# Kernel optimization log

Measured on AMD Instinct MI355X. Metric: run time of the kernel, lower is better.

Reference implementation:

```python
import jax, jax.numpy as jnp
import numpy as np
import math

D_MODEL = 1024
N_HEADS = 16
D_K = D_MODEL // N_HEADS
LN_EPS = 1e-5


def _linear_params(key, d_in, d_out):
    # torch Linear stores weight as [out, in]; xavier_uniform init
    bound = math.sqrt(6.0 / (d_in + d_out))
    kw, kb = jax.random.split(key)
    W = jax.random.uniform(kw, (d_out, d_in), jnp.float32, -bound, bound)
    b = jnp.zeros((d_out,), jnp.float32)
    return W, b


def setup_inputs() -> dict:
    key = jax.random.key(0)
    ks = jax.random.split(key, 8)
    x = jax.random.normal(ks[0], (2, 2048, D_MODEL), jnp.float32)
    reasoning_state = jax.random.normal(ks[1], (2, D_MODEL), jnp.float32)
    Wq, bq = _linear_params(ks[2], D_MODEL, D_MODEL)
    Wk, bk = _linear_params(ks[3], D_MODEL, D_MODEL)
    Wv, bv = _linear_params(ks[4], D_MODEL, D_MODEL)
    Wr, br = _linear_params(ks[5], D_MODEL, D_MODEL)
    Wo, bo = _linear_params(ks[6], D_MODEL, D_MODEL)
    ln_g = jnp.ones((D_MODEL,), jnp.float32)
    ln_b = jnp.zeros((D_MODEL,), jnp.float32)
    return {"x": x, "reasoning_state": reasoning_state,
            "Wq": Wq, "bq": bq, "Wk": Wk, "bk": bk, "Wv": Wv, "bv": bv,
            "Wr": Wr, "br": br, "Wo": Wo, "bo": bo, "ln_g": ln_g, "ln_b": ln_b}


def reference(x, reasoning_state, Wq, bq, Wk, bk, Wv, bv, Wr, br, Wo, bo, ln_g, ln_b):
    B, S, D = x.shape
    H, dk = N_HEADS, D_K

    def proj(z, W, b):  # torch Linear: z @ W.T + b
        return z @ W.T + b

    # [B, H, S, dk]
    Q = proj(x, Wq, bq).reshape(B, S, H, dk).transpose(0, 2, 1, 3)
    K = proj(x, Wk, bk).reshape(B, S, H, dk).transpose(0, 2, 1, 3)
    V = proj(x, Wv, bv).reshape(B, S, H, dk).transpose(0, 2, 1, 3)

    scores = jnp.einsum('bhsd,bhtd->bhst', Q, K) / math.sqrt(dk)

    # reasoning bias: R is [B, H, 1, dk]; Q @ R^T -> [B, H, S, 1], broadcast over keys
    R = proj(reasoning_state, Wr, br).reshape(B, 1, H, dk).transpose(0, 2, 1, 3)
    scores = scores + jnp.einsum('bhsd,bhud->bhsu', Q, R)  # u == 1, broadcasts

    attn = jax.nn.softmax(scores, axis=-1)
    context = jnp.einsum('bhst,bhtd->bshd', attn, V).reshape(B, S, D)
    out = proj(context, Wo, bo)

    # residual + LayerNorm
    y = out + x
    mu = jnp.mean(y, axis=-1, keepdims=True)
    var = jnp.var(y, axis=-1, keepdims=True)
    y = (y - mu) * jax.lax.rsqrt(var + LN_EPS) * ln_g + ln_b
    return (y, attn)
```

## Files before the change

### kernel.cpp

```cpp
#include <hip/hip_runtime.h>
#include <hip/hip_bf16.h>

#define DM 1024
#define NH 16
#define DKK 64
#define SL 2048
#define NBATCH 2
#define NR (NBATCH*SL)

typedef __attribute__((ext_vector_type(8))) __bf16 bf16x8;
typedef __attribute__((ext_vector_type(4))) float f32x4;
using bf16 = __hip_bfloat16;

#define QSCALE 0.18033688011112042f

__global__ __launch_bounds__(256) void cvt5_kernel(
    const float* __restrict__ sx, const float* __restrict__ s1,
    const float* __restrict__ s2, const float* __restrict__ s3, const float* __restrict__ s4,
    bf16* __restrict__ dx, bf16* __restrict__ d1,
    bf16* __restrict__ d2, bf16* __restrict__ d3, bf16* __restrict__ d4) {
  const int z = blockIdx.y;
  const float* src = (z == 0) ? sx : (z == 1) ? s1 : (z == 2) ? s2 : (z == 3) ? s3 : s4;
  bf16* dst = (z == 0) ? dx : (z == 1) ? d1 : (z == 2) ? d2 : (z == 3) ? d3 : d4;
  const int n4 = (z == 0) ? (NR * DM / 4) : (DM * DM / 4);
  int stride = gridDim.x * blockDim.x;
  for (int i = blockIdx.x * blockDim.x + threadIdx.x; i < n4; i += stride) {
    float4 v = ((const float4*)src)[i];
    union { bf16 h[4]; ushort4 u; } un;
    un.h[0] = __float2bfloat16(v.x);
    un.h[1] = __float2bfloat16(v.y);
    un.h[2] = __float2bfloat16(v.z);
    un.h[3] = __float2bfloat16(v.w);
    ((ushort4*)dst)[i] = un.u;
  }
}

__global__ __launch_bounds__(256) void gemm_qkv_kernel(
    const bf16* __restrict__ xb,
    const bf16* __restrict__ Wqb, const bf16* __restrict__ Wkb, const bf16* __restrict__ Wvb,
    const float* __restrict__ bq, const float* __restrict__ bk, const float* __restrict__ bv,
    bf16* __restrict__ Qb, bf16* __restrict__ Kb, bf16* __restrict__ Vt) {
  __shared__ bf16 smem[8192];
  bf16* As = smem;
  bf16* Bs = smem + 4096;
  const int z = blockIdx.z;
  const bf16* W = (z == 0) ? Wqb : (z == 1) ? Wkb : Wvb;
  const float* bias = (z == 0) ? bq : (z == 1) ? bk : bv;
  const int rowStart = blockIdx.y * 128, colStart = blockIdx.x * 64;
  const int t = threadIdx.x, lane = t & 63, w = t >> 6;
  const int lg = lane & 15, lh = lane >> 4;
  const int wm = (w >> 1) * 64, wn = (w & 1) * 32;

  f32x4 acc[4][2];
#pragma unroll
  for (int i = 0; i < 4; ++i)
#pragma unroll
    for (int j = 0; j < 2; ++j) acc[i][j] = (f32x4){0.f, 0.f, 0.f, 0.f};

  for (int kt = 0; kt < DM / 32; ++kt) {
    int kb = kt * 32;
#pragma unroll
    for (int q = 0; q < 2; ++q) {
      int idx = q * 256 + t;
      int row = idx >> 2;
      int ce = (idx & 3) * 8;
      const bf16* ga = xb + (size_t)(rowStart + row) * DM + kb + ce;
      int ldsbase = (q * 256 + w * 64) * 8;
      __builtin_amdgcn_global_load_lds((const __attribute__((address_space(1))) void*)ga,
                                       (__attribute__((address_space(3))) void*)(As + ldsbase),
                                       16, 0, 0);
    }
    {
      int row = t >> 2, ce = (t & 3) * 8;
      const bf16* gb = W + (size_t)(colStart + row) * DM + kb + ce;
      int ldsbase = (w * 64) * 8;
      __builtin_amdgcn_global_load_lds((const __attribute__((address_space(1))) void*)gb,
                                       (__attribute__((address_space(3))) void*)(Bs + ldsbase),
                                       16, 0, 0);
    }
    __syncthreads();
    bf16x8 af[4], bfr[2];
#pragma unroll
    for (int i = 0; i < 4; ++i)
      af[i] = *(const bf16x8*)(As + (wm + i * 16 + lg) * 32 + 8 * lh);
#pragma unroll
    for (int j = 0; j < 2; ++j)
      bfr[j] = *(const bf16x8*)(Bs + (wn + j * 16 + lg) * 32 + 8 * lh);
#pragma unroll
    for (int i = 0; i < 4; ++i)
#pragma unroll
      for (int j = 0; j < 2; ++j)
        acc[i][j] = __builtin_amdgcn_mfma_f32_16x16x32_bf16(af[i], bfr[j], acc[i][j], 0, 0, 0);
    __syncthreads();
  }

  if (z < 2) {
    bf16* out = (z == 0) ? Qb : Kb;
    const float sc = (z == 0) ? QSCALE : 1.0f;
#pragma unroll
    for (int i = 0; i < 4; ++i)
#pragma unroll
      for (int j = 0; j < 2; ++j) {
        int col = colStart + wn + j * 16 + lg;
        float bb = bias[col];
#pragma unroll
        for (int r = 0; r < 4; ++r) {
          int row = rowStart + wm + i * 16 + 4 * lh + r;
          out[(size_t)row * DM + col] = __float2bfloat16((acc[i][j][r] + bb) * sc);
        }
      }
  } else {
    char* T = (char*)smem;
    __syncthreads();
#pragma unroll
    for (int i = 0; i < 4; ++i)
#pragma unroll
      for (int j = 0; j < 2; ++j) {
        int col = wn + j * 16 + lg;
        float bb = bias[colStart + col];
        const int swz = (col & 7) << 4;
#pragma unroll
        for (int r2 = 0; r2 < 4; r2 += 2) {
          int row = wm + i * 16 + 4 * lh + r2;
          union { bf16 hh[2]; unsigned u; } un;
          un.hh[0] = __float2bfloat16(acc[i][j][r2] + bb);
          un.hh[1] = __float2bfloat16(acc[i][j][r2 + 1] + bb);
          *(unsigned*)(T + ((col * 256 + row * 2) ^ swz)) = un.u;
        }
      }
    __syncthreads();
    const int b_i = rowStart >> 11;
    const int sbase = rowStart & 2047;
#pragma unroll
    for (int rd = 0; rd < 4; ++rd) {
      int d_loc = rd * 16 + (t >> 4);
      int s8 = (t & 15) * 8;
      bf16x8 v = *(const bf16x8*)(T + ((d_loc * 256 + s8 * 2) ^ ((d_loc & 7) << 4)));
      int col = colStart + d_loc;
      int h2 = col >> 6, d = col & 63;
      *(bf16x8*)(Vt + ((size_t)(b_i * NH + h2) * DKK + d) * SL + sbase + s8) = v;
    }
  }
}

__global__ __launch_bounds__(256) void attn_den_kernel(
    const bf16* __restrict__ Qb, const bf16* __restrict__ Kb,
    float* __restrict__ linv_g) {
  __shared__ float sl[2 * 128];
  const int t = threadIdx.x, lane = t & 63, w = t >> 6;
  const int lg = lane & 15, lh = lane >> 4;
  const int L = blockIdx.x;
  const int xcd = L & 7, s_in = L >> 3;
  const int bh = xcd * 4 + (s_in >> 4);
  const int qtile = s_in & 15;
  const int b = bh >> 4, h = bh & 15;
  const int qbase = qtile * 128;
  const int wr = w >> 1, wc = w & 1;

  bf16x8 qf[4][2];
#pragma unroll
  for (int i = 0; i < 4; ++i)
#pragma unroll
    for (int ks = 0; ks < 2; ++ks)
      qf[i][ks] = *(const bf16x8*)(Qb +
          (size_t)(b * SL + qbase + wr * 64 + i * 16 + lg) * DM + h * DKK + ks * 32 + 8 * lh);

  const bf16* Kbase = Kb + (size_t)b * SL * DM + h * DKK;

  float lsum[4] = {0.f, 0.f, 0.f, 0.f};
  for (int kt = 0; kt < 16; ++kt) {
    bf16x8 kf[4][2];
#pragma unroll
    for (int j = 0; j < 4; ++j)
#pragma unroll
      for (int ks = 0; ks < 2; ++ks)
        kf[j][ks] = *(const bf16x8*)(Kbase +
            (size_t)(kt * 128 + wc * 64 + j * 16 + lg) * DM + ks * 32 + 8 * lh);
#pragma unroll
    for (int i = 0; i < 4; ++i) {
      f32x4 s[4];
#pragma unroll
      for (int j = 0; j < 4; ++j) {
        f32x4 z = (f32x4){0.f, 0.f, 0.f, 0.f};
        z = __builtin_amdgcn_mfma_f32_16x16x32_bf16(kf[j][0], qf[i][0], z, 0, 0, 0);
        s[j] = __builtin_amdgcn_mfma_f32_16x16x32_bf16(kf[j][1], qf[i][1], z, 0, 0, 0);
      }
#pragma unroll
      for (int j = 0; j < 4; ++j)
#pragma unroll
        for (int r = 0; r < 4; ++r) lsum[i] += exp2f(s[j][r]);
    }
  }
#pragma unroll
  for (int i = 0; i < 4; ++i) {
    lsum[i] += __shfl_xor(lsum[i], 16);
    lsum[i] += __shfl_xor(lsum[i], 32);
  }
  if (lh == 0) {
#pragma unroll
    for (int i = 0; i < 4; ++i) sl[wc * 128 + wr * 64 + i * 16 + lg] = lsum[i];
  }
  __syncthreads();
  if (t < 128) {
    linv_g[(size_t)bh * SL + qbase + t] = 1.f / (sl[t] + sl[128 + t]);
  }
}

__global__ __launch_bounds__(256) void attn_wr_kernel(
    const bf16* __restrict__ Qb, const bf16* __restrict__ Kb, const bf16* __restrict__ Vt,
    const float* __restrict__ linv_g,
    float* __restrict__ attn_out, bf16* __restrict__ ctxb) {
  __shared__ bf16 Ps[4][2][32 * 128];
  const int t = threadIdx.x, lane = t & 63, w = t >> 6;
  const int lg = lane & 15, lh = lane >> 4;
  const int L = blockIdx.x;
  const int xcd = L & 7, s_in = L >> 3;
  const int bh = xcd * 4 + (s_in >> 4);
  const int qtile = s_in & 15;
  const int b = bh >> 4, h = bh & 15;
  const int qb2 = qtile * 128 + w * 32;
  char* Pw = (char*)(&Ps[w][0][0]);

  bf16x8 qf[2][2];
#pragma unroll
  for (int i = 0; i < 2; ++i)
#pragma unroll
    for (int ks = 0; ks < 2; ++ks)
      qf[i][ks] = *(const bf16x8*)(Qb +
          (size_t)(b * SL + qb2 + i * 16 + lg) * DM + h * DKK + ks * 32 + 8 * lh);

  float linv[2];
#pragma unroll
  for (int i = 0; i < 2; ++i)
    linv[i] = linv_g[(size_t)bh * SL + qb2 + i * 16 + lg];

  const bf16* Kbase = Kb + (size_t)b * SL * DM + h * DKK;
  const bf16* Vtb = Vt + (size_t)bh * DKK * SL;
  float* attn_base = attn_out + (size_t)bh * SL * SL;

  f32x4 cacc[2][4];
#pragma unroll
  for (int i = 0; i < 2; ++i)
#pragma unroll
    for (int jd = 0; jd < 4; ++jd) cacc[i][jd] = (f32x4){0.f, 0.f, 0.f, 0.f};

  for (int kt = 0; kt < 16; ++kt) {
    char* Pb = Pw + (kt & 1) * 8192;
    bf16x8 kf[8][2];
#pragma unroll
    for (int j = 0; j < 8; ++j)
#pragma unroll
      for (int ks = 0; ks < 2; ++ks)
        kf[j][ks] = *(const bf16x8*)(Kbase +
            (size_t)(kt * 128 + j * 16 + lg) * DM + ks * 32 + 8 * lh);
    bf16x8 vfall[4][4];
#pragma unroll
    for (int ks = 0; ks < 4; ++ks)
#pragma unroll
      for (int jd = 0; jd < 4; ++jd)
        vfall[ks][jd] = *(const bf16x8*)(Vtb +
            (size_t)(jd * 16 + lg) * SL + kt * 128 + ks * 32 + 8 * lh);

#pragma unroll
    for (int i = 0; i < 2; ++i) {
      f32x4 s[8];
      __builtin_amdgcn_s_setprio(1);
#pragma unroll
      for (int j = 0; j < 8; ++j) {
        f32x4 z = (f32x4){0.f, 0.f, 0.f, 0.f};
        z = __builtin_amdgcn_mfma_f32_16x16x32_bf16(kf[j][0], qf[i][0], z, 0, 0, 0);
        s[j] = __builtin_amdgcn_mfma_f32_16x16x32_bf16(kf[j][1], qf[i][1], z, 0, 0, 0);
      }
      __builtin_amdgcn_s_setprio(0);
      const int qloc = i * 16 + lg;
      const int swz = (qloc & 7) << 4;
#pragma unroll
      for (int j = 0; j < 8; ++j) {
        const int key0 = j * 16 + 4 * lh;
        f32x4 p4;
        p4[0] = exp2f(s[j][0]) * linv[i];
        p4[1] = exp2f(s[j][1]) * linv[i];
        p4[2] = exp2f(s[j][2]) * linv[i];
        p4[3] = exp2f(s[j][3]) * linv[i];
        __builtin_nontemporal_store(p4,
            (f32x4*)(attn_base + (size_t)(qb2 + qloc) * SL + kt * 128 + key0));
        union { bf16 hh[4]; ushort4 u4; } un;
        un.hh[0] = __float2bfloat16(p4[0]);
        un.hh[1] = __float2bfloat16(p4[1]);
        un.hh[2] = __float2bfloat16(p4[2]);
        un.hh[3] = __float2bfloat16(p4[3]);
        *(ushort4*)(Pb + ((qloc * 256 + key0 * 2) ^ swz)) = un.u4;
      }
    }

    __builtin_amdgcn_s_setprio(1);
#pragma unroll
    for (int ks = 0; ks < 4; ++ks) {
      bf16x8 pf[2];
#pragma unroll
      for (int i = 0; i < 2; ++i) {
        const int qloc = i * 16 + lg;
        pf[i] = *(const bf16x8*)(Pb + ((qloc * 256 + (ks * 32 + 8 * lh) * 2) ^ ((qloc & 7) << 4)));
      }
#pragma unroll
      for (int i = 0; i < 2; ++i)
#pragma unroll
        for (int jd = 0; jd < 4; ++jd)
          cacc[i][jd] = __builtin_amdgcn_mfma_f32_16x16x32_bf16(pf[i], vfall[ks][jd], cacc[i][jd], 0, 0, 0);
    }
    __builtin_amdgcn_s_setprio(0);
  }

#pragma unroll
  for (int i = 0; i < 2; ++i)
#pragma unroll
    for (int jd = 0; jd < 4; ++jd)
#pragma unroll
      for (int r = 0; r < 4; ++r) {
        int row = qb2 + i * 16 + 4 * lh + r;
        int d = jd * 16 + lg;
        ctxb[(size_t)(b * SL + row) * DM + h * DKK + d] = __float2bfloat16(cacc[i][jd][r]);
      }
}

__global__ __launch_bounds__(256) void gemm_o_kernel(
    const bf16* __restrict__ ctxb, const bf16* __restrict__ Wob, const float* __restrict__ bo,
    const float* __restrict__ xf, float* __restrict__ ypre) {
  __shared__ bf16 As[128 * 32], Bs[64 * 32];
  const int t = threadIdx.x, lane = t & 63, w = t >> 6;
  const int lg = lane & 15, lh = lane >> 4;
  const int wm = (w >> 1) * 64, wn = (w & 1) * 32;
  int rowStart = blockIdx.y * 128, colStart = blockIdx.x * 64;
  f32x4 acc[4][2];
#pragma unroll
  for (int i = 0; i < 4; ++i)
#pragma unroll
    for (int j = 0; j < 2; ++j) acc[i][j] = (f32x4){0.f, 0.f, 0.f, 0.f};

  for (int kt = 0; kt < DM / 32; ++kt) {
    int kb = kt * 32;
#pragma unroll
    for (int q = 0; q < 2; ++q) {
      int idx = q * 256 + t;
      int row = idx >> 2;
      int ce = (idx & 3) * 8;
      const bf16* ga = ctxb + (size_t)(rowStart + row) * DM + kb + ce;
      int ldsbase = (q * 256 + w * 64) * 8;
      __builtin_amdgcn_global_load_lds((const __attribute__((address_space(1))) void*)ga,
                                       (__attribute__((address_space(3))) void*)(As + ldsbase),
                                       16, 0, 0);
    }
    {
      int row = t >> 2, ce = (t & 3) * 8;
      const bf16* gb = Wob + (size_t)(colStart + row) * DM + kb + ce;
      int ldsbase = (w * 64) * 8;
      __builtin_amdgcn_global_load_lds((const __attribute__((address_space(1))) void*)gb,
                                       (__attribute__((address_space(3))) void*)(Bs + ldsbase),
                                       16, 0, 0);
    }
    __syncthreads();
    bf16x8 af[4], bfr[2];
#pragma unroll
    for (int i = 0; i < 4; ++i)
      af[i] = *(const bf16x8*)(As + (wm + i * 16 + lg) * 32 + 8 * lh);
#pragma unroll
    for (int j = 0; j < 2; ++j)
      bfr[j] = *(const bf16x8*)(Bs + (wn + j * 16 + lg) * 32 + 8 * lh);
#pragma unroll
    for (int i = 0; i < 4; ++i)
#pragma unroll
      for (int j = 0; j < 2; ++j)
        acc[i][j] = __builtin_amdgcn_mfma_f32_16x16x32_bf16(af[i], bfr[j], acc[i][j], 0, 0, 0);
    __syncthreads();
  }
#pragma unroll
  for (int i = 0; i < 4; ++i)
#pragma unroll
    for (int j = 0; j < 2; ++j) {
      int col = colStart + wn + j * 16 + lg;
      float bb = bo[col];
#pragma unroll
      for (int r = 0; r < 4; ++r) {
        int row = rowStart + wm + i * 16 + 4 * lh + r;
        ypre[(size_t)row * DM + col] = acc[i][j][r] + bb + xf[(size_t)row * DM + col];
      }
    }
}

__global__ __launch_bounds__(256) void ln_kernel(const float* __restrict__ ypre,
                                                 const float* __restrict__ g,
                                                 const float* __restrict__ bta,
                                                 float* __restrict__ out) {
  int row = blockIdx.x;
  const float* yr = ypre + (size_t)row * DM;
  int t = threadIdx.x;
  float4 v = *(const float4*)(yr + t * 4);
  float s = v.x + v.y + v.z + v.w;
  float ss = v.x * v.x + v.y * v.y + v.z * v.z + v.w * v.w;
#pragma unroll
  for (int off = 1; off < 64; off <<= 1) {
    s += __shfl_xor(s, off);
    ss += __shfl_xor(ss, off);
  }
  __shared__ float red[8];
  int w = t >> 6, lane = t & 63;
  if (lane == 0) { red[w] = s; red[4 + w] = ss; }
  __syncthreads();
  s = red[0] + red[1] + red[2] + red[3];
  ss = red[4] + red[5] + red[6] + red[7];
  float mu = s * (1.f / (float)DM);
  float var = ss * (1.f / (float)DM) - mu * mu;
  float rstd = rsqrtf(var + 1e-5f);
  float4 gv = *(const float4*)(g + t * 4);
  float4 bv = *(const float4*)(bta + t * 4);
  float4 o;
  o.x = (v.x - mu) * rstd * gv.x + bv.x;
  o.y = (v.y - mu) * rstd * gv.y + bv.y;
  o.z = (v.z - mu) * rstd * gv.z + bv.z;
  o.w = (v.w - mu) * rstd * gv.w + bv.w;
  *(float4*)(out + (size_t)row * DM + t * 4) = o;
}

extern "C" void kernel_launch(void* const* d_in, const int* in_sizes, int n_in,
                              void* d_out, int out_size, void* d_ws, size_t ws_size,
                              hipStream_t stream) {
  (void)in_sizes; (void)n_in; (void)out_size; (void)ws_size;
  const float* x = (const float*)d_in[0];
  const float* Wq = (const float*)d_in[2];
  const float* bq = (const float*)d_in[3];
  const float* Wk = (const float*)d_in[4];
  const float* bk = (const float*)d_in[5];
  const float* Wv = (const float*)d_in[6];
  const float* bv = (const float*)d_in[7];
  const float* Wo = (const float*)d_in[10];
  const float* bo = (const float*)d_in[11];
  const float* ln_g = (const float*)d_in[12];
  const float* ln_b = (const float*)d_in[13];
  float* out = (float*)d_out;

  char* ws = (char*)d_ws;
  const size_t MB = 1ull << 20;
  bf16* xb   = (bf16*)(ws + 0 * MB);
  bf16* Wqb  = (bf16*)(ws + 8 * MB);
  bf16* Wkb  = (bf16*)(ws + 10 * MB);
  bf16* Wvb  = (bf16*)(ws + 12 * MB);
  bf16* Wob  = (bf16*)(ws + 14 * MB);
  bf16* Qb   = (bf16*)(ws + 16 * MB);
  bf16* Kb   = (bf16*)(ws + 24 * MB);
  bf16* Vt   = (bf16*)(ws + 32 * MB);
  bf16* ctxb = (bf16*)(ws + 40 * MB);
  float* ypre = (float*)(ws + 48 * MB);
  float* linv_g = (float*)(ws + 64 * MB);

  float* y_out = out;
  float* attn_out = out + (size_t)NR * DM;

  cvt5_kernel<<<dim3(512, 5), 256, 0, stream>>>(x, Wq, Wk, Wv, Wo, xb, Wqb, Wkb, Wvb, Wob);

  gemm_qkv_kernel<<<dim3(16, 32, 3), 256, 0, stream>>>(xb, Wqb, Wkb, Wvb, bq, bk, bv, Qb, Kb, Vt);
  attn_den_kernel<<<512, 256, 0, stream>>>(Qb, Kb, linv_g);
  attn_wr_kernel<<<512, 256, 0, stream>>>(Qb, Kb, Vt, linv_g, attn_out, ctxb);
  gemm_o_kernel<<<dim3(16, 32), 256, 0, stream>>>(ctxb, Wob, bo, x, ypre);
  ln_kernel<<<4096, 256, 0, stream>>>(ypre, ln_g, ln_b, y_out);
}
```

Measured before the change: 303.2 us.

## Fold softmax denominator into PV kernel and split attention-prob write into its own kernel

The separate denominator pass is removed. The context kernel now accumulates exp-sums alongside the unnormalized PV product, normalizes the context at the end and stores the reciprocal sums. A new store-only kernel recomputes QK^T with a finer grid of 1024 blocks and streams the normalized fp32 attention matrix. This aims to take the large attention-matrix stores out of the MFMA-heavy PV loop so each kernel is either compute-bound or purely bandwidth-bound. The cost is that the store kernel no longer overlaps with PV compute.

New measurement: 371.8 us. +22.6%, slower.

```diff
diff --git a/kernel.cpp b/kernel.cpp
--- a/kernel.cpp
+++ b/kernel.cpp
@@ -143,74 +143,11 @@
   }
 }
 
-__global__ __launch_bounds__(256) void attn_den_kernel(
-    const bf16* __restrict__ Qb, const bf16* __restrict__ Kb,
-    float* __restrict__ linv_g) {
-  __shared__ float sl[2 * 128];
-  const int t = threadIdx.x, lane = t & 63, w = t >> 6;
-  const int lg = lane & 15, lh = lane >> 4;
-  const int L = blockIdx.x;
-  const int xcd = L & 7, s_in = L >> 3;
-  const int bh = xcd * 4 + (s_in >> 4);
-  const int qtile = s_in & 15;
-  const int b = bh >> 4, h = bh & 15;
-  const int qbase = qtile * 128;
-  const int wr = w >> 1, wc = w & 1;
-
-  bf16x8 qf[4][2];
-#pragma unroll
-  for (int i = 0; i < 4; ++i)
-#pragma unroll
-    for (int ks = 0; ks < 2; ++ks)
-      qf[i][ks] = *(const bf16x8*)(Qb +
-          (size_t)(b * SL + qbase + wr * 64 + i * 16 + lg) * DM + h * DKK + ks * 32 + 8 * lh);
-
-  const bf16* Kbase = Kb + (size_t)b * SL * DM + h * DKK;
-
-  float lsum[4] = {0.f, 0.f, 0.f, 0.f};
-  for (int kt = 0; kt < 16; ++kt) {
-    bf16x8 kf[4][2];
-#pragma unroll
-    for (int j = 0; j < 4; ++j)
-#pragma unroll
-      for (int ks = 0; ks < 2; ++ks)
-        kf[j][ks] = *(const bf16x8*)(Kbase +
-            (size_t)(kt * 128 + wc * 64 + j * 16 + lg) * DM + ks * 32 + 8 * lh);
-#pragma unroll
-    for (int i = 0; i < 4; ++i) {
-      f32x4 s[4];
-#pragma unroll
-      for (int j = 0; j < 4; ++j) {
-        f32x4 z = (f32x4){0.f, 0.f, 0.f, 0.f};
-        z = __builtin_amdgcn_mfma_f32_16x16x32_bf16(kf[j][0], qf[i][0], z, 0, 0, 0);
-        s[j] = __builtin_amdgcn_mfma_f32_16x16x32_bf16(kf[j][1], qf[i][1], z, 0, 0, 0);
-      }
-#pragma unroll
-      for (int j = 0; j < 4; ++j)
-#pragma unroll
-        for (int r = 0; r < 4; ++r) lsum[i] += exp2f(s[j][r]);
-    }
-  }
-#pragma unroll
-  for (int i = 0; i < 4; ++i) {
-    lsum[i] += __shfl_xor(lsum[i], 16);
-    lsum[i] += __shfl_xor(lsum[i], 32);
-  }
-  if (lh == 0) {
-#pragma unroll
-    for (int i = 0; i < 4; ++i) sl[wc * 128 + wr * 64 + i * 16 + lg] = lsum[i];
-  }
-  __syncthreads();
-  if (t < 128) {
-    linv_g[(size_t)bh * SL + qbase + t] = 1.f / (sl[t] + sl[128 + t]);
-  }
-}
-
-__global__ __launch_bounds__(256) void attn_wr_kernel(
+__global__ __launch_bounds__(256) void attn_ctx_kernel(
     const bf16* __restrict__ Qb, const bf16* __restrict__ Kb, const bf16* __restrict__ Vt,
-    const float* __restrict__ linv_g,
-    float* __restrict__ attn_out, bf16* __restrict__ ctxb) {
+    float* __restrict__ linv_g, bf16* __restrict__ ctxb) {
   __shared__ bf16 Ps[4][2][32 * 128];
+  __shared__ float lssh[4][32];
   const int t = threadIdx.x, lane = t & 63, w = t >> 6;
   const int lg = lane & 15, lh = lane >> 4;
   const int L = blockIdx.x;
@@ -229,20 +166,15 @@
       qf[i][ks] = *(const bf16x8*)(Qb +
           (size_t)(b * SL + qb2 + i * 16 + lg) * DM + h * DKK + ks * 32 + 8 * lh);
 
-  float linv[2];
-#pragma unroll
-  for (int i = 0; i < 2; ++i)
-    linv[i] = linv_g[(size_t)bh * SL + qb2 + i * 16 + lg];
-
   const bf16* Kbase = Kb + (size_t)b * SL * DM + h * DKK;
   const bf16* Vtb = Vt + (size_t)bh * DKK * SL;
-  float* attn_base = attn_out + (size_t)bh * SL * SL;
 
   f32x4 cacc[2][4];
 #pragma unroll
   for (int i = 0; i < 2; ++i)
 #pragma unroll
     for (int jd = 0; jd < 4; ++jd) cacc[i][jd] = (f32x4){0.f, 0.f, 0.f, 0.f};
+  float lsum[2] = {0.f, 0.f};
 
   for (int kt = 0; kt < 16; ++kt) {
     char* Pb = Pw + (kt & 1) * 8192;
@@ -277,18 +209,16 @@
 #pragma unroll
       for (int j = 0; j < 8; ++j) {
         const int key0 = j * 16 + 4 * lh;
-        f32x4 p4;
-        p4[0] = exp2f(s[j][0]) * linv[i];
-        p4[1] = exp2f(s[j][1]) * linv[i];
-        p4[2] = exp2f(s[j][2]) * linv[i];
-        p4[3] = exp2f(s[j][3]) * linv[i];
-        __builtin_nontemporal_store(p4,
-            (f32x4*)(attn_base + (size_t)(qb2 + qloc) * SL + kt * 128 + key0));
+        float p0 = exp2f(s[j][0]);
+        float p1 = exp2f(s[j][1]);
+        float p2 = exp2f(s[j][2]);
+        float p3 = exp2f(s[j][3]);
+        lsum[i] += (p0 + p1) + (p2 + p3);
         union { bf16 hh[4]; ushort4 u4; } un;
-        un.hh[0] = __float2bfloat16(p4[0]);
-        un.hh[1] = __float2bfloat16(p4[1]);
-        un.hh[2] = __float2bfloat16(p4[2]);
-        un.hh[3] = __float2bfloat16(p4[3]);
+        un.hh[0] = __float2bfloat16(p0);
+        un.hh[1] = __float2bfloat16(p1);
+        un.hh[2] = __float2bfloat16(p2);
+        un.hh[3] = __float2bfloat16(p3);
         *(ushort4*)(Pb + ((qloc * 256 + key0 * 2) ^ swz)) = un.u4;
       }
     }
@@ -312,15 +242,81 @@
   }
 
 #pragma unroll
+  for (int i = 0; i < 2; ++i) {
+    lsum[i] += __shfl_xor(lsum[i], 16);
+    lsum[i] += __shfl_xor(lsum[i], 32);
+  }
+  float linv[2];
+#pragma unroll
+  for (int i = 0; i < 2; ++i) linv[i] = 1.f / lsum[i];
+  if (lh == 0) {
+#pragma unroll
+    for (int i = 0; i < 2; ++i) {
+      linv_g[(size_t)bh * SL + qb2 + i * 16 + lg] = linv[i];
+      lssh[w][i * 16 + lg] = linv[i];
+    }
+  }
+  asm volatile("s_waitcnt lgkmcnt(0)" ::: "memory");
+
+#pragma unroll
   for (int i = 0; i < 2; ++i)
 #pragma unroll
     for (int jd = 0; jd < 4; ++jd)
 #pragma unroll
       for (int r = 0; r < 4; ++r) {
-        int row = qb2 + i * 16 + 4 * lh + r;
+        int rloc = i * 16 + 4 * lh + r;
+        int row = qb2 + rloc;
         int d = jd * 16 + lg;
-        ctxb[(size_t)(b * SL + row) * DM + h * DKK + d] = __float2bfloat16(cacc[i][jd][r]);
-      }
+        ctxb[(size_t)(b * SL + row) * DM + h * DKK + d] =
+            __float2bfloat16(cacc[i][jd][r] * lssh[w][rloc]);
+      }
+}
+
+__global__ __launch_bounds__(256) void attn_write_kernel(
+    const bf16* __restrict__ Qb, const bf16* __restrict__ Kb,
+    const float* __restrict__ linv_g, float* __restrict__ attn_out) {
+  const int t = threadIdx.x, lane = t & 63, w = t >> 6;
+  const int lg = lane & 15, lh = lane >> 4;
+  const int L = blockIdx.x;
+  const int xcd = L & 7, s_in = L >> 3;
+  const int bh = xcd * 4 + (s_in >> 5);
+  const int qtile = s_in & 31;
+  const int b = bh >> 4, h = bh & 15;
+  const int qb2 = qtile * 64 + w * 16;
+
+  bf16x8 qf[2];
+#pragma unroll
+  for (int ks = 0; ks < 2; ++ks)
+    qf[ks] = *(const bf16x8*)(Qb +
+        (size_t)(b * SL + qb2 + lg) * DM + h * DKK + ks * 32 + 8 * lh);
+  const float linv = linv_g[(size_t)bh * SL + qb2 + lg];
+
+  const bf16* Kbase = Kb + (size_t)b * SL * DM + h * DKK;
+  float* rowbase = attn_out + (size_t)bh * SL * SL + (size_t)(qb2 + lg) * SL;
+
+  for (int kt = 0; kt < 16; ++kt) {
+    bf16x8 kf[8][2];
+#pragma unroll
+    for (int j = 0; j < 8; ++j)
+#pragma unroll
+      for (int ks = 0; ks < 2; ++ks)
+        kf[j][ks] = *(const bf16x8*)(Kbase +
+            (size_t)(kt * 128 + j * 16 + lg) * DM + ks * 32 + 8 * lh);
+    __builtin_amdgcn_s_setprio(1);
+#pragma unroll
+    for (int j = 0; j < 8; ++j) {
+      f32x4 z = (f32x4){0.f, 0.f, 0.f, 0.f};
+      z = __builtin_amdgcn_mfma_f32_16x16x32_bf16(kf[j][0], qf[0], z, 0, 0, 0);
+      f32x4 s = __builtin_amdgcn_mfma_f32_16x16x32_bf16(kf[j][1], qf[1], z, 0, 0, 0);
+      f32x4 p4;
+      p4[0] = exp2f(s[0]) * linv;
+      p4[1] = exp2f(s[1]) * linv;
+      p4[2] = exp2f(s[2]) * linv;
+      p4[3] = exp2f(s[3]) * linv;
+      __builtin_nontemporal_store(p4, (f32x4*)(rowbase + kt * 128 + j * 16 + 4 * lh));
+    }
+    __builtin_amdgcn_s_setprio(0);
+  }
 }
 
 __global__ __launch_bounds__(256) void gemm_o_kernel(
@@ -458,8 +454,8 @@
   cvt5_kernel<<<dim3(512, 5), 256, 0, stream>>>(x, Wq, Wk, Wv, Wo, xb, Wqb, Wkb, Wvb, Wob);
 
   gemm_qkv_kernel<<<dim3(16, 32, 3), 256, 0, stream>>>(xb, Wqb, Wkb, Wvb, bq, bk, bv, Qb, Kb, Vt);
-  attn_den_kernel<<<512, 256, 0, stream>>>(Qb, Kb, linv_g);
-  attn_wr_kernel<<<512, 256, 0, stream>>>(Qb, Kb, Vt, linv_g, attn_out, ctxb);
+  attn_ctx_kernel<<<512, 256, 0, stream>>>(Qb, Kb, Vt, linv_g, ctxb);
+  attn_write_kernel<<<1024, 256, 0, stream>>>(Qb, Kb, linv_g, attn_out);
   gemm_o_kernel<<<dim3(16, 32), 256, 0, stream>>>(ctxb, Wob, bo, x, ypre);
   ln_kernel<<<4096, 256, 0, stream>>>(ypre, ln_g, ln_b, y_out);
 }
```
